# Kernel tuning notes

Measured on AMD Instinct MI355X. Metric: run time of the kernel, lower is better.

## Reference

```python
import jax, jax.numpy as jnp
import numpy as np

NUM_USER, NUM_ITEM, NUM_TAG, K = 100000, 1000000, 100000, 64
B = 1048576


def setup_inputs() -> dict:
    key = jax.random.key(0)
    ks = jax.random.split(key, 8)
    lim = np.sqrt(3.0 / K).astype(np.float32)
    return {
        "x": jax.random.randint(ks[0], (B, 4), 0, NUM_USER, dtype=jnp.int64) if jax.config.jax_enable_x64 else jax.random.randint(ks[0], (B, 4), 0, NUM_USER, dtype=jnp.int32),
        "user_vecs": jax.random.normal(ks[1], (NUM_USER, K), dtype=jnp.float32) * 0.01,
        "item_vecs": jax.random.normal(ks[2], (NUM_ITEM, K), dtype=jnp.float32) * 0.01,
        "tag_vecs": jax.random.normal(ks[3], (NUM_TAG, K), dtype=jnp.float32) * 0.01,
        "w_user": jax.random.uniform(ks[4], (K, K), jnp.float32, -lim, lim),
        "b_user": jnp.zeros((K,), jnp.float32),
        "w_item": jax.random.uniform(ks[5], (K, K), jnp.float32, -lim, lim),
        "b_item": jnp.zeros((K,), jnp.float32),
    }


def reference(x, user_vecs, item_vecs, tag_vecs, w_user, b_user, w_item, b_item):
    # gathers: [B, K]
    user_vec = user_vecs[x[:, 0]]
    item_vec = item_vecs[x[:, 1]]
    tag_vec = tag_vecs[x[:, 2]]
    neg_tag_vec = tag_vecs[x[:, 3]]
    # nn.Linear: y = t @ W.T + b, then sigmoid
    ut = jax.nn.sigmoid(tag_vec @ w_user.T + b_user)
    it = jax.nn.sigmoid(tag_vec @ w_item.T + b_item)
    nut = jax.nn.sigmoid(neg_tag_vec @ w_user.T + b_user)
    nit = jax.nn.sigmoid(neg_tag_vec @ w_item.T + b_item)
    r = (jnp.sum(user_vec * ut, axis=1) + jnp.sum(item_vec * it, axis=1)
         - (jnp.sum(user_vec * nut, axis=1) + jnp.sum(item_vec * nit, axis=1)))
    return r
```

## Files before the change

### kernel.cpp

```cpp
#include <hip/hip_runtime.h>
#include <hip/hip_fp16.h>


__device__ __forceinline__ float sigmoidf_(float z) {
    return 1.0f / (1.0f + __expf(-z));
}

__device__ __forceinline__ int h2_as_int(__half2 h) {
    union { __half2 h; int i; } u; u.h = h; return u.i;
}
__device__ __forceinline__ __half2 int_as_h2(int i) {
    union { __half2 h; int i; } u; u.i = i; return u.h;
}

__global__ __launch_bounds__(256) void precompute_tags(
    const float* __restrict__ tag_vecs,
    const float* __restrict__ w_user, const float* __restrict__ b_user,
    const float* __restrict__ w_item, const float* __restrict__ b_item,
    int4* __restrict__ C, int num_tag)
{
    __shared__ float wu[64 * 64];
    __shared__ float wi[64 * 64];
    __shared__ float bu[64];
    __shared__ float bi[64];

    for (int i = threadIdx.x; i < 1024; i += 256) {
        ((float4*)wu)[i] = ((const float4*)w_user)[i];
        ((float4*)wi)[i] = ((const float4*)w_item)[i];
    }
    if (threadIdx.x < 64) {
        bu[threadIdx.x] = b_user[threadIdx.x];
        bi[threadIdx.x] = b_item[threadIdx.x];
    }
    __syncthreads();

    int tag = blockIdx.x * 256 + threadIdx.x;
    if (tag >= num_tag) return;

    float4 tv[16];
    const float4* tp = (const float4*)(tag_vecs + (size_t)tag * 64);
    #pragma unroll
    for (int k = 0; k < 16; ++k) tv[k] = tp[k];

    int4* crow = C + (size_t)tag * 16;

    #pragma unroll 2
    for (int c = 0; c < 16; ++c) {
        float d0, d1, d2, d3, e0, e1, e2, e3;
        float* dd[4] = {&d0, &d1, &d2, &d3};
        float* ee[4] = {&e0, &e1, &e2, &e3};
        #pragma unroll
        for (int jj = 0; jj < 4; ++jj) {
            int j = 4 * c + jj;
            float au = bu[j];
            float ai = bi[j];
            const float4* wur = (const float4*)(wu + j * 64);
            const float4* wir = (const float4*)(wi + j * 64);
            #pragma unroll
            for (int k = 0; k < 16; ++k) {
                float4 a = wur[k];
                float4 b = wir[k];
                float4 t = tv[k];
                au += t.x * a.x + t.y * a.y + t.z * a.z + t.w * a.w;
                ai += t.x * b.x + t.y * b.y + t.z * b.z + t.w * b.w;
            }
            *dd[jj] = sigmoidf_(au) - 0.5f;
            *ee[jj] = sigmoidf_(ai) - 0.5f;
        }
        int4 pack;
        pack.x = h2_as_int(__floats2half2_rn(d0, d1));
        pack.y = h2_as_int(__floats2half2_rn(d2, d3));
        pack.z = h2_as_int(__floats2half2_rn(e0, e1));
        pack.w = h2_as_int(__floats2half2_rn(e2, e3));
        crow[c] = pack;
    }
}

__global__ __launch_bounds__(256) void convert_fp16(
    const float* __restrict__ user_vecs,
    const float* __restrict__ item_vecs,
    int2* __restrict__ U16, int2* __restrict__ I16,
    int nu4, int ni4)
{
    int tid = blockIdx.x * 256 + threadIdx.x;
    int stride = gridDim.x * 256;
    int total = nu4 + ni4;
    for (int i = tid; i < total; i += stride) {
        float4 v;
        int2* dst;
        if (i < nu4) { v = ((const float4*)user_vecs)[i]; dst = U16 + i; }
        else         { v = ((const float4*)item_vecs)[i - nu4]; dst = I16 + (i - nu4); }
        int2 h;
        h.x = h2_as_int(__floats2half2_rn(v.x, v.y));
        h.y = h2_as_int(__floats2half2_rn(v.z, v.w));
        *dst = h;
    }
}

__global__ __launch_bounds__(256) void score_kernel(
    const int* __restrict__ x,
    const int2* __restrict__ U16,
    const int2* __restrict__ I16,
    const float* __restrict__ item_vecs,
    const int4* __restrict__ C,
    float* __restrict__ out, int B, int n_hot)
{
    int sub = threadIdx.x & 15;
    int row0 = (blockIdx.x * 256 + threadIdx.x) >> 4;
    int rstride = (gridDim.x * 256) >> 4;

    for (int row = row0; row < B; row += rstride) {
        int4 idx = ((const int4*)x)[row];

        int2 uh = U16[(size_t)idx.x * 16 + sub];
        int4 ct = C[(size_t)idx.z * 16 + sub];
        int4 cn = C[(size_t)idx.w * 16 + sub];

        float2 u01 = __half22float2(int_as_h2(uh.x));
        float2 u23 = __half22float2(int_as_h2(uh.y));

        float2 i01, i23;
        if (idx.y < n_hot) {
            int2 ih = I16[(size_t)idx.y * 16 + sub];
            i01 = __half22float2(int_as_h2(ih.x));
            i23 = __half22float2(int_as_h2(ih.y));
        } else {
            float4 ivf = ((const float4*)(item_vecs + (size_t)idx.y * 64))[sub];
            i01 = make_float2(ivf.x, ivf.y);
            i23 = make_float2(ivf.z, ivf.w);
        }

        float2 dt01 = __half22float2(int_as_h2(ct.x));
        float2 dt23 = __half22float2(int_as_h2(ct.y));
        float2 et01 = __half22float2(int_as_h2(ct.z));
        float2 et23 = __half22float2(int_as_h2(ct.w));
        float2 dn01 = __half22float2(int_as_h2(cn.x));
        float2 dn23 = __half22float2(int_as_h2(cn.y));
        float2 en01 = __half22float2(int_as_h2(cn.z));
        float2 en23 = __half22float2(int_as_h2(cn.w));

        float p = u01.x * (dt01.x - dn01.x) + u01.y * (dt01.y - dn01.y)
                + u23.x * (dt23.x - dn23.x) + u23.y * (dt23.y - dn23.y)
                + i01.x * (et01.x - en01.x) + i01.y * (et01.y - en01.y)
                + i23.x * (et23.x - en23.x) + i23.y * (et23.y - en23.y);

        p += __shfl_xor(p, 1);
        p += __shfl_xor(p, 2);
        p += __shfl_xor(p, 4);
        p += __shfl_xor(p, 8);

        if (sub == 0) __builtin_nontemporal_store(p, out + row);
    }
}

__global__ __launch_bounds__(256) void fused_fallback(
    const int* __restrict__ x,
    const float* __restrict__ user_vecs,
    const float* __restrict__ item_vecs,
    const float* __restrict__ tag_vecs,
    const float* __restrict__ w_user, const float* __restrict__ b_user,
    const float* __restrict__ w_item, const float* __restrict__ b_item,
    float* __restrict__ out, int B)
{
    int tid = blockIdx.x * 256 + threadIdx.x;
    int row = tid >> 6;
    int lane = tid & 63;
    if (row >= B) return;

    int4 idx = ((const int4*)x)[row];

    float t  = tag_vecs[(size_t)idx.z * 64 + lane];
    float nt = tag_vecs[(size_t)idx.w * 64 + lane];

    const float* wur = w_user + lane * 64;
    const float* wir = w_item + lane * 64;

    float zu = b_user[lane], zi = b_item[lane];
    float nzu = zu, nzi = zi;
    #pragma unroll 8
    for (int k = 0; k < 64; ++k) {
        float tk  = __shfl(t, k, 64);
        float ntk = __shfl(nt, k, 64);
        float wuk = wur[k];
        float wik = wir[k];
        zu  += tk * wuk;  zi  += tk * wik;
        nzu += ntk * wuk; nzi += ntk * wik;
    }

    float ut  = sigmoidf_(zu);
    float itg = sigmoidf_(zi);
    float nut = sigmoidf_(nzu);
    float nit = sigmoidf_(nzi);

    float uv  = user_vecs[(size_t)idx.x * 64 + lane];
    float ivv = item_vecs[(size_t)idx.y * 64 + lane];
    float p = uv * (ut - nut) + ivv * (itg - nit);

    #pragma unroll
    for (int off = 32; off; off >>= 1) p += __shfl_xor(p, off, 64);

    if (lane == 0) out[row] = p;
}

extern "C" void kernel_launch(void* const* d_in, const int* in_sizes, int n_in,
                              void* d_out, int out_size, void* d_ws, size_t ws_size,
                              hipStream_t stream) {
    const int*   x         = (const int*)d_in[0];
    const float* user_vecs = (const float*)d_in[1];
    const float* item_vecs = (const float*)d_in[2];
    const float* tag_vecs  = (const float*)d_in[3];
    const float* w_user    = (const float*)d_in[4];
    const float* b_user    = (const float*)d_in[5];
    const float* w_item    = (const float*)d_in[6];
    const float* b_item    = (const float*)d_in[7];
    float* out = (float*)d_out;

    const int B        = in_sizes[0] / 4;
    const int num_user = in_sizes[1] / 64;
    const int num_item = in_sizes[2] / 64;
    const int num_tag  = in_sizes[3] / 64;
    const int n_hot    = (num_item < num_user) ? num_item : num_user;

    const size_t bytes_C = (size_t)num_tag * 256;
    const size_t bytes_U = (size_t)num_user * 128;
    const size_t bytes_I = (size_t)n_hot * 128;
    const size_t need = bytes_C + bytes_U + bytes_I;

    if (ws_size >= need) {
        int4* C   = (int4*)d_ws;
        int2* U16 = (int2*)((char*)d_ws + bytes_C);
        int2* I16 = (int2*)((char*)d_ws + bytes_C + bytes_U);

        precompute_tags<<<(num_tag + 255) / 256, 256, 0, stream>>>(
            tag_vecs, w_user, b_user, w_item, b_item, C, num_tag);

        int nu4 = num_user * 16;
        int ni4 = n_hot * 16;
        int cblocks = (nu4 + ni4 + 255) / 256;
        if (cblocks > 2048) cblocks = 2048;
        convert_fp16<<<cblocks, 256, 0, stream>>>(
            user_vecs, item_vecs, U16, I16, nu4, ni4);

        int nblocks = (B * 16 + 255) / 256;
        if (nblocks > 65536) nblocks = 65536;
        score_kernel<<<nblocks, 256, 0, stream>>>(
            x, U16, I16, item_vecs, C, out, B, n_hot);
    } else {
        fused_fallback<<<((size_t)B * 64 + 255) / 256, 256, 0, stream>>>(
            x, user_vecs, item_vecs, tag_vecs,
            w_user, b_user, w_item, b_item, out, B);
    }
}
```

Baseline: 508.0 us.

## Merge tag precompute and fp16 conversion into one kernel; two rows per group

Merges the tag-projection precompute and the user/item fp16 conversion into a single launch, with separate block ranges doing each job so the two run concurrently. Each tag thread now computes two tags so every shared-memory weight read is reused twice. The score kernel handles two rows per 16-lane group, issuing both rows' gathers before any arithmetic to raise memory-level parallelism. The costs are higher register pressure (launch_bounds 256,1, doubled tv arrays) and fewer tag blocks, which may reduce occupancy.

```diff
diff --git a/kernel.cpp b/kernel.cpp
--- a/kernel.cpp
+++ b/kernel.cpp
@@ -13,12 +13,38 @@
     union { __half2 h; int i; } u; u.i = i; return u.h;
 }
 
-__global__ __launch_bounds__(256) void precompute_tags(
+#define TAG_BLOCKS_T(nt)  (((nt) + 511) / 512)
+
+__global__ __launch_bounds__(256, 1) void prep_kernel(
     const float* __restrict__ tag_vecs,
     const float* __restrict__ w_user, const float* __restrict__ b_user,
     const float* __restrict__ w_item, const float* __restrict__ b_item,
-    int4* __restrict__ C, int num_tag)
+    const float* __restrict__ user_vecs,
+    const float* __restrict__ item_vecs,
+    int4* __restrict__ C, int2* __restrict__ U16, int2* __restrict__ I16,
+    int num_tag, int nu4, int ni4)
 {
+    const int tag_blocks = TAG_BLOCKS_T(num_tag);
+
+    if ((int)blockIdx.x >= tag_blocks) {
+        int cb = blockIdx.x - tag_blocks;
+        int nconv_blocks = gridDim.x - tag_blocks;
+        int tid = cb * 256 + threadIdx.x;
+        int stride = nconv_blocks * 256;
+        int total = nu4 + ni4;
+        for (int i = tid; i < total; i += stride) {
+            float4 v;
+            int2* dst;
+            if (i < nu4) { v = ((const float4*)user_vecs)[i]; dst = U16 + i; }
+            else         { v = ((const float4*)item_vecs)[i - nu4]; dst = I16 + (i - nu4); }
+            int2 h;
+            h.x = h2_as_int(__floats2half2_rn(v.x, v.y));
+            h.y = h2_as_int(__floats2half2_rn(v.z, v.w));
+            *dst = h;
+        }
+        return;
+    }
+
     __shared__ float wu[64 * 64];
     __shared__ float wi[64 * 64];
     __shared__ float bu[64];
@@ -34,66 +60,61 @@
     }
     __syncthreads();
 
-    int tag = blockIdx.x * 256 + threadIdx.x;
-    if (tag >= num_tag) return;
-
-    float4 tv[16];
-    const float4* tp = (const float4*)(tag_vecs + (size_t)tag * 64);
-    #pragma unroll
-    for (int k = 0; k < 16; ++k) tv[k] = tp[k];
-
-    int4* crow = C + (size_t)tag * 16;
-
-    #pragma unroll 2
+    int tag0 = blockIdx.x * 512 + threadIdx.x;
+    int tag1 = tag0 + 256;
+    bool ok0 = tag0 < num_tag;
+    bool ok1 = tag1 < num_tag;
+    if (!ok0) return;
+
+    float4 tv0[16], tv1[16];
+    {
+        const float4* tp0 = (const float4*)(tag_vecs + (size_t)tag0 * 64);
+        const float4* tp1 = (const float4*)(tag_vecs + (size_t)(ok1 ? tag1 : tag0) * 64);
+        #pragma unroll
+        for (int k = 0; k < 16; ++k) { tv0[k] = tp0[k]; tv1[k] = tp1[k]; }
+    }
+
+    int4* crow0 = C + (size_t)tag0 * 16;
+    int4* crow1 = C + (size_t)(ok1 ? tag1 : tag0) * 16;
+
     for (int c = 0; c < 16; ++c) {
-        float d0, d1, d2, d3, e0, e1, e2, e3;
-        float* dd[4] = {&d0, &d1, &d2, &d3};
-        float* ee[4] = {&e0, &e1, &e2, &e3};
+        float d0[4], e0[4], d1[4], e1[4];
         #pragma unroll
         for (int jj = 0; jj < 4; ++jj) {
             int j = 4 * c + jj;
-            float au = bu[j];
-            float ai = bi[j];
+            float au0 = bu[j], ai0 = bi[j];
+            float au1 = au0,  ai1 = ai0;
             const float4* wur = (const float4*)(wu + j * 64);
             const float4* wir = (const float4*)(wi + j * 64);
             #pragma unroll
             for (int k = 0; k < 16; ++k) {
                 float4 a = wur[k];
                 float4 b = wir[k];
-                float4 t = tv[k];
-                au += t.x * a.x + t.y * a.y + t.z * a.z + t.w * a.w;
-                ai += t.x * b.x + t.y * b.y + t.z * b.z + t.w * b.w;
+                float4 t0 = tv0[k];
+                float4 t1 = tv1[k];
+                au0 += t0.x * a.x + t0.y * a.y + t0.z * a.z + t0.w * a.w;
+                ai0 += t0.x * b.x + t0.y * b.y + t0.z * b.z + t0.w * b.w;
+                au1 += t1.x * a.x + t1.y * a.y + t1.z * a.z + t1.w * a.w;
+                ai1 += t1.x * b.x + t1.y * b.y + t1.z * b.z + t1.w * b.w;
             }
-            *dd[jj] = sigmoidf_(au) - 0.5f;
-            *ee[jj] = sigmoidf_(ai) - 0.5f;
-        }
-        int4 pack;
-        pack.x = h2_as_int(__floats2half2_rn(d0, d1));
-        pack.y = h2_as_int(__floats2half2_rn(d2, d3));
-        pack.z = h2_as_int(__floats2half2_rn(e0, e1));
-        pack.w = h2_as_int(__floats2half2_rn(e2, e3));
-        crow[c] = pack;
-    }
-}
-
-__global__ __launch_bounds__(256) void convert_fp16(
-    const float* __restrict__ user_vecs,
-    const float* __restrict__ item_vecs,
-    int2* __restrict__ U16, int2* __restrict__ I16,
-    int nu4, int ni4)
-{
-    int tid = blockIdx.x * 256 + threadIdx.x;
-    int stride = gridDim.x * 256;
-    int total = nu4 + ni4;
-    for (int i = tid; i < total; i += stride) {
-        float4 v;
-        int2* dst;
-        if (i < nu4) { v = ((const float4*)user_vecs)[i]; dst = U16 + i; }
-        else         { v = ((const float4*)item_vecs)[i - nu4]; dst = I16 + (i - nu4); }
-        int2 h;
-        h.x = h2_as_int(__floats2half2_rn(v.x, v.y));
-        h.y = h2_as_int(__floats2half2_rn(v.z, v.w));
-        *dst = h;
+            d0[jj] = sigmoidf_(au0) - 0.5f;
+            e0[jj] = sigmoidf_(ai0) - 0.5f;
+            d1[jj] = sigmoidf_(au1) - 0.5f;
+            e1[jj] = sigmoidf_(ai1) - 0.5f;
+        }
+        int4 p0, p1;
+        p0.x = h2_as_int(__floats2half2_rn(d0[0], d0[1]));
+        p0.y = h2_as_int(__floats2half2_rn(d0[2], d0[3]));
+        p0.z = h2_as_int(__floats2half2_rn(e0[0], e0[1]));
+        p0.w = h2_as_int(__floats2half2_rn(e0[2], e0[3]));
+        crow0[c] = p0;
+        if (ok1) {
+            p1.x = h2_as_int(__floats2half2_rn(d1[0], d1[1]));
+            p1.y = h2_as_int(__floats2half2_rn(d1[2], d1[3]));
+            p1.z = h2_as_int(__floats2half2_rn(e1[0], e1[1]));
+            p1.w = h2_as_int(__floats2half2_rn(e1[2], e1[3]));
+            crow1[c] = p1;
+        }
     }
 }
 
@@ -106,50 +127,88 @@
     float* __restrict__ out, int B, int n_hot)
 {
     int sub = threadIdx.x & 15;
-    int row0 = (blockIdx.x * 256 + threadIdx.x) >> 4;
-    int rstride = (gridDim.x * 256) >> 4;
-
-    for (int row = row0; row < B; row += rstride) {
-        int4 idx = ((const int4*)x)[row];
-
-        int2 uh = U16[(size_t)idx.x * 16 + sub];
-        int4 ct = C[(size_t)idx.z * 16 + sub];
-        int4 cn = C[(size_t)idx.w * 16 + sub];
-
-        float2 u01 = __half22float2(int_as_h2(uh.x));
-        float2 u23 = __half22float2(int_as_h2(uh.y));
-
-        float2 i01, i23;
-        if (idx.y < n_hot) {
-            int2 ih = I16[(size_t)idx.y * 16 + sub];
-            i01 = __half22float2(int_as_h2(ih.x));
-            i23 = __half22float2(int_as_h2(ih.y));
+    int grp0 = (blockIdx.x * 256 + threadIdx.x) >> 4;
+    int gstride = (gridDim.x * 256) >> 4;
+
+    for (int grp = grp0; grp * 2 < B; grp += gstride) {
+        int rowA = grp * 2;
+        int rowB = rowA + 1;
+        bool hasB = rowB < B;
+
+        int4 ia = ((const int4*)x)[rowA];
+        int4 ib = ((const int4*)x)[hasB ? rowB : rowA];
+
+        int2 uhA = U16[(size_t)ia.x * 16 + sub];
+        int4 ctA = C[(size_t)ia.z * 16 + sub];
+        int4 cnA = C[(size_t)ia.w * 16 + sub];
+        int2 uhB = U16[(size_t)ib.x * 16 + sub];
+        int4 ctB = C[(size_t)ib.z * 16 + sub];
+        int4 cnB = C[(size_t)ib.w * 16 + sub];
+
+        float2 iA01, iA23, iB01, iB23;
+        if (ia.y < n_hot) {
+            int2 ih = I16[(size_t)ia.y * 16 + sub];
+            iA01 = __half22float2(int_as_h2(ih.x));
+            iA23 = __half22float2(int_as_h2(ih.y));
         } else {
-            float4 ivf = ((const float4*)(item_vecs + (size_t)idx.y * 64))[sub];
-            i01 = make_float2(ivf.x, ivf.y);
-            i23 = make_float2(ivf.z, ivf.w);
-        }
-
-        float2 dt01 = __half22float2(int_as_h2(ct.x));
-        float2 dt23 = __half22float2(int_as_h2(ct.y));
-        float2 et01 = __half22float2(int_as_h2(ct.z));
-        float2 et23 = __half22float2(int_as_h2(ct.w));
-        float2 dn01 = __half22float2(int_as_h2(cn.x));
-        float2 dn23 = __half22float2(int_as_h2(cn.y));
-        float2 en01 = __half22float2(int_as_h2(cn.z));
-        float2 en23 = __half22float2(int_as_h2(cn.w));
-
-        float p = u01.x * (dt01.x - dn01.x) + u01.y * (dt01.y - dn01.y)
-                + u23.x * (dt23.x - dn23.x) + u23.y * (dt23.y - dn23.y)
-                + i01.x * (et01.x - en01.x) + i01.y * (et01.y - en01.y)
-                + i23.x * (et23.x - en23.x) + i23.y * (et23.y - en23.y);
-
-        p += __shfl_xor(p, 1);
-        p += __shfl_xor(p, 2);
-        p += __shfl_xor(p, 4);
-        p += __shfl_xor(p, 8);
-
-        if (sub == 0) __builtin_nontemporal_store(p, out + row);
+            float4 f = ((const float4*)(item_vecs + (size_t)ia.y * 64))[sub];
+            iA01 = make_float2(f.x, f.y); iA23 = make_float2(f.z, f.w);
+        }
+        if (ib.y < n_hot) {
+            int2 ih = I16[(size_t)ib.y * 16 + sub];
+            iB01 = __half22float2(int_as_h2(ih.x));
+            iB23 = __half22float2(int_as_h2(ih.y));
+        } else {
+            float4 f = ((const float4*)(item_vecs + (size_t)ib.y * 64))[sub];
+            iB01 = make_float2(f.x, f.y); iB23 = make_float2(f.z, f.w);
+        }
+
+        {
+            float2 u01 = __half22float2(int_as_h2(uhA.x));
+            float2 u23 = __half22float2(int_as_h2(uhA.y));
+            float2 dt01 = __half22float2(int_as_h2(ctA.x));
+            float2 dt23 = __half22float2(int_as_h2(ctA.y));
+            float2 et01 = __half22float2(int_as_h2(ctA.z));
+            float2 et23 = __half22float2(int_as_h2(ctA.w));
+            float2 dn01 = __half22float2(int_as_h2(cnA.x));
+            float2 dn23 = __half22float2(int_as_h2(cnA.y));
+            float2 en01 = __half22float2(int_as_h2(cnA.z));
+            float2 en23 = __half22float2(int_as_h2(cnA.w));
+
+            float p = u01.x * (dt01.x - dn01.x) + u01.y * (dt01.y - dn01.y)
+                    + u23.x * (dt23.x - dn23.x) + u23.y * (dt23.y - dn23.y)
+                    + iA01.x * (et01.x - en01.x) + iA01.y * (et01.y - en01.y)
+                    + iA23.x * (et23.x - en23.x) + iA23.y * (et23.y - en23.y);
+
+            p += __shfl_xor(p, 1);
+            p += __shfl_xor(p, 2);
+            p += __shfl_xor(p, 4);
+            p += __shfl_xor(p, 8);
+            if (sub == 0) __builtin_nontemporal_store(p, out + rowA);
+        }
+        if (hasB) {
+            float2 u01 = __half22float2(int_as_h2(uhB.x));
+            float2 u23 = __half22float2(int_as_h2(uhB.y));
+            float2 dt01 = __half22float2(int_as_h2(ctB.x));
+            float2 dt23 = __half22float2(int_as_h2(ctB.y));
+            float2 et01 = __half22float2(int_as_h2(ctB.z));
+            float2 et23 = __half22float2(int_as_h2(ctB.w));
+            float2 dn01 = __half22float2(int_as_h2(cnB.x));
+            float2 dn23 = __half22float2(int_as_h2(cnB.y));
+            float2 en01 = __half22float2(int_as_h2(cnB.z));
+            float2 en23 = __half22float2(int_as_h2(cnB.w));
+
+            float p = u01.x * (dt01.x - dn01.x) + u01.y * (dt01.y - dn01.y)
+                    + u23.x * (dt23.x - dn23.x) + u23.y * (dt23.y - dn23.y)
+                    + iB01.x * (et01.x - en01.x) + iB01.y * (et01.y - en01.y)
+                    + iB23.x * (et23.x - en23.x) + iB23.y * (et23.y - en23.y);
+
+            p += __shfl_xor(p, 1);
+            p += __shfl_xor(p, 2);
+            p += __shfl_xor(p, 4);
+            p += __shfl_xor(p, 8);
+            if (sub == 0) __builtin_nontemporal_store(p, out + rowB);
+        }
     }
 }
 
@@ -231,18 +290,19 @@
         int2* U16 = (int2*)((char*)d_ws + bytes_C);
         int2* I16 = (int2*)((char*)d_ws + bytes_C + bytes_U);
 
-        precompute_tags<<<(num_tag + 255) / 256, 256, 0, stream>>>(
-            tag_vecs, w_user, b_user, w_item, b_item, C, num_tag);
-
         int nu4 = num_user * 16;
         int ni4 = n_hot * 16;
-        int cblocks = (nu4 + ni4 + 255) / 256;
-        if (cblocks > 2048) cblocks = 2048;
-        convert_fp16<<<cblocks, 256, 0, stream>>>(
-            user_vecs, item_vecs, U16, I16, nu4, ni4);
-
-        int nblocks = (B * 16 + 255) / 256;
-        if (nblocks > 65536) nblocks = 65536;
+        int tag_blocks = TAG_BLOCKS_T(num_tag);
+        int conv_blocks = (nu4 + ni4 + 255) / 256;
+        if (conv_blocks > 1024) conv_blocks = 1024;
+
+        prep_kernel<<<tag_blocks + conv_blocks, 256, 0, stream>>>(
+            tag_vecs, w_user, b_user, w_item, b_item,
+            user_vecs, item_vecs, C, U16, I16, num_tag, nu4, ni4);
+
+        int ngrp = (B + 1) / 2;
+        int nblocks = (ngrp * 16 + 255) / 256;
+        if (nblocks > 32768) nblocks = 32768;
         score_kernel<<<nblocks, 256, 0, stream>>>(
             x, U16, I16, item_vecs, C, out, B, n_hot);
     } else {
```

Result: slower. 668.3 us (+31.6%).
